# Kernel optimization log

Hardware: AMD Instinct MI355X
Metric: run time of the kernel (lower is better)

Reference implementation:

```python
import jax, jax.numpy as jnp
from jax import lax
import numpy as np

B, L, D = 2, 2048, 768
DI, DS, DTR, K = 1536, 16, 48, 4  # d_inner, d_state, dt_rank, d_conv
EPS = 1e-5


def layernorm(x, g, b):
    mu = jnp.mean(x, axis=-1, keepdims=True)
    var = jnp.mean(jnp.square(x - mu), axis=-1, keepdims=True)
    return (x - mu) * lax.rsqrt(var + EPS) * g + b


def mamba(x, in_w, conv_w, conv_b, xproj_w, dt_w, dt_b, A_log, Dp, out_w):
    # x: [B, L, D]
    xz = x @ in_w.T                       # [B, L, 2*DI]
    xc, z = jnp.split(xz, 2, axis=-1)     # [B, L, DI] each
    # causal depthwise conv1d, kernel K, left pad K-1, truncate to L
    xp = jnp.pad(xc, ((0, 0), (K - 1, 0), (0, 0)))
    conv = conv_b + sum(xp[:, k:k + L, :] * conv_w[:, k] for k in range(K))
    xc = jax.nn.silu(conv)
    dbc = xc @ xproj_w.T                  # [B, L, DTR+2*DS]
    dt = dbc[..., :DTR]
    Bm = dbc[..., DTR:DTR + DS]           # [B, L, DS]
    Cm = dbc[..., DTR + DS:]              # [B, L, DS]
    dt = jax.nn.softplus(dt @ dt_w.T + dt_b)  # [B, L, DI]
    A = -jnp.exp(A_log)                   # [DI, DS]

    def step(h, inp):
        dt_t, B_t, C_t, x_t = inp         # [B,DI], [B,DS], [B,DS], [B,DI]
        dA = jnp.exp(dt_t[..., None] * A)               # [B, DI, DS]
        h = dA * h + (dt_t * x_t)[..., None] * B_t[:, None, :]
        y = jnp.einsum('bds,bs->bd', h, C_t)
        return h, y

    h0 = jnp.zeros((x.shape[0], DI, DS), x.dtype)
    _, ys = lax.scan(step, h0, (dt.transpose(1, 0, 2), Bm.transpose(1, 0, 2),
                                Cm.transpose(1, 0, 2), xc.transpose(1, 0, 2)))
    y = ys.transpose(1, 0, 2) + xc * Dp   # [B, L, DI]
    y = y * jax.nn.silu(z)
    return y @ out_w.T                    # [B, L, D]


def setup_inputs() -> dict:
    key = jax.random.key(0)
    ks = iter(jax.random.split(key, 40))
    r = lambda s, sc=0.02: jax.random.normal(next(ks), s, jnp.float32) * sc
    A0 = jnp.log(jnp.broadcast_to(jnp.arange(1, DS + 1, dtype=jnp.float32), (DI, DS)))
    def mamba_params(p):
        return {
            f'{p}_in_w': r((2 * DI, D)), f'{p}_conv_w': r((DI, K), 0.2),
            f'{p}_conv_b': jnp.zeros((DI,)), f'{p}_xproj_w': r((DTR + 2 * DS, DI)),
            f'{p}_dt_w': r((DI, DTR), 0.1), f'{p}_dt_b': jnp.zeros((DI,)),
            f'{p}_A_log': A0, f'{p}_D': jnp.ones((DI,)), f'{p}_out_w': r((D, DI)),
        }
    inp = {'x': jax.random.normal(next(ks), (B, L, D), jnp.float32),
           'norm_g': jnp.ones((D,)), 'norm_b': jnp.zeros((D,))}
    inp.update(mamba_params('f'))
    inp.update(mamba_params('b'))
    inp.update({'mix_w': r((D, 2 * D)), 'mix_b': jnp.zeros((D,)),
                'ffn_w1': r((4 * D, D)), 'ffn_b1': jnp.zeros((4 * D,)),
                'ffn_w2': r((D, 4 * D)), 'ffn_b2': jnp.zeros((D,)),
                'ffn_norm_g': jnp.ones((D,)), 'ffn_norm_b': jnp.zeros((D,))})
    return inp


def reference(x, norm_g, norm_b,
              f_in_w, f_conv_w, f_conv_b, f_xproj_w, f_dt_w, f_dt_b, f_A_log, f_D, f_out_w,
              b_in_w, b_conv_w, b_conv_b, b_xproj_w, b_dt_w, b_dt_b, b_A_log, b_D, b_out_w,
              mix_w, mix_b, ffn_w1, ffn_b1, ffn_w2, ffn_b2, ffn_norm_g, ffn_norm_b):
    residual = x
    xn = layernorm(x, norm_g, norm_b)
    xf = mamba(xn, f_in_w, f_conv_w, f_conv_b, f_xproj_w, f_dt_w, f_dt_b, f_A_log, f_D, f_out_w)
    xb = mamba(jnp.flip(xn, axis=1), b_in_w, b_conv_w, b_conv_b, b_xproj_w,
               b_dt_w, b_dt_b, b_A_log, b_D, b_out_w)
    xb = jnp.flip(xb, axis=1)
    xm = jnp.concatenate([xf, xb], axis=-1) @ mix_w.T + mix_b
    h = xm + residual
    hn = layernorm(h, ffn_norm_g, ffn_norm_b)
    ff = jax.nn.gelu(hn @ ffn_w1.T + ffn_b1) @ ffn_w2.T + ffn_b2  # dropout = eval identity
    return ff + h
```

## Files before the change

kernel.cpp:

```cpp
#include <hip/hip_runtime.h>
#include <hip/hip_bf16.h>
#include <math.h>

#define NB 2
#define LL 2048
#define DD 768
#define DI 1536
#define DS 16
#define MM (NB*LL)
#define TCH 64
#define NCH 32

typedef __hip_bfloat16 bf16;
typedef __attribute__((ext_vector_type(8))) __bf16 bf16x8;
typedef __attribute__((ext_vector_type(4))) float f32x4;

__device__ __forceinline__ float b2f(bf16 v){ return __bfloat162float(v); }
__device__ __forceinline__ bf16 f2b(float v){ return __float2bfloat16(v); }

__device__ __forceinline__ void un2(unsigned u, float& lo, float& hi){
  union {unsigned i; float f;} a, b;
  a.i = u << 16; b.i = u & 0xffff0000u;
  lo = a.f; hi = b.f;
}

__device__ __forceinline__ void async_cp16(const bf16* g, __bf16* l) {
  __builtin_amdgcn_global_load_lds((const __attribute__((address_space(1))) void*)g,
                                   (__attribute__((address_space(3))) void*)l, 16, 0, 0);
}

#define ACT_NONE 0
#define ACT_SOFTPLUS 1
#define ACT_GELU 2

__device__ __forceinline__ float apply_act(float v, int act) {
  if (act == ACT_SOFTPLUS) {
    v = (v > 15.f) ? v : log1pf(__expf(v));
  } else if (act == ACT_GELU) {
    float u = 0.7978845608028654f * (v + 0.044715f*v*v*v);
    v = 0.5f * v * (1.f + tanhf(u));
  }
  return v;
}

__global__ void gemm_kernel(const bf16* __restrict__ A, int lda,
                            const bf16* __restrict__ B, int ldb,
                            void* __restrict__ C, int ldc,
                            int N, int K,
                            const float* __restrict__ bias,
                            const float* __restrict__ addp, int ldadd,
                            int act, int f32out)
{
  __shared__ __bf16 As[128*64];
  __shared__ __bf16 Bs[128*64];
  const int tid  = threadIdx.x;
  const int lane = tid & 63, wave = tid >> 6;
  const int m0 = blockIdx.x * 128, n0 = blockIdx.y * 128;
  const int wm = wave & 1, wn = wave >> 1;

  const int srow = wave*32 + (lane >> 3);
  const int gsw  = (lane & 7) ^ ((lane >> 3) & 7);
  const int scol = gsw * 8;
  const bf16* Ag[4]; const bf16* Bg[4];
  __bf16 *AsW[4], *BsW[4];
  #pragma unroll
  for (int i = 0; i < 4; i++) {
    int ar = m0 + srow + i*8;
    Ag[i] = A + (size_t)ar * lda + scol;
    int br = n0 + srow + i*8; if (br > N-1) br = N-1;
    Bg[i] = B + (size_t)br * ldb + scol;
    AsW[i] = &As[(wave*32 + i*8)*64];
    BsW[i] = &Bs[(wave*32 + i*8)*64];
  }

  f32x4 acc[4][4] = {};
  const int arow = wm*64 + (lane & 15);
  const int brow = wn*64 + (lane & 15);
  const int rx = lane & 7;
  const int gq = lane >> 4;

  for (int kb = 0; kb < K; kb += 64) {
    __syncthreads();
    #pragma unroll
    for (int i = 0; i < 4; i++) {
      async_cp16(Ag[i] + kb, AsW[i]);
      async_cp16(Bg[i] + kb, BsW[i]);
    }
    __syncthreads();
    #pragma unroll
    for (int h = 0; h < 2; h++) {
      const int kk = ((h*4 + gq) ^ rx) * 8;
      bf16x8 af[4], bfr[4];
      #pragma unroll
      for (int i = 0; i < 4; i++) af[i]  = *(const bf16x8*)&As[(arow + i*16)*64 + kk];
      #pragma unroll
      for (int j = 0; j < 4; j++) bfr[j] = *(const bf16x8*)&Bs[(brow + j*16)*64 + kk];
      #pragma unroll
      for (int i = 0; i < 4; i++)
        #pragma unroll
        for (int j = 0; j < 4; j++)
          acc[i][j] = __builtin_amdgcn_mfma_f32_16x16x32_bf16(af[i], bfr[j], acc[i][j], 0, 0, 0);
    }
  }

  bf16*  Cb = (bf16*)C;
  float* Cf = (float*)C;
  #pragma unroll
  for (int i = 0; i < 4; i++) {
    int rbase = m0 + wm*64 + i*16 + (lane >> 4)*4;
    #pragma unroll
    for (int j = 0; j < 4; j++) {
      int col = n0 + wn*64 + j*16 + (lane & 15);
      if (col >= N) continue;
      float bv = bias ? bias[col] : 0.f;
      #pragma unroll
      for (int r = 0; r < 4; r++) {
        int row = rbase + r;
        float v = apply_act(acc[i][j][r] + bv, act);
        if (addp) v += addp[(size_t)row * ldadd + col];
        if (f32out) Cf[(size_t)row * ldc + col] = v;
        else        Cb[(size_t)row * ldc + col] = f2b(v);
      }
    }
  }
}

__global__ void gemm64_kernel(const bf16* __restrict__ A, int lda, size_t sA,
                              const bf16* __restrict__ B, int ldb, size_t sB,
                              void* __restrict__ C, int ldc, size_t sC,
                              int N, int K,
                              const float* __restrict__ bias0,
                              const float* __restrict__ bias1, int biasBase,
                              const float* __restrict__ addp, int ldadd,
                              int act, int f32out)
{
  __shared__ __bf16 As[64*64];
  __shared__ __bf16 Bs[64*64];
  const int tid  = threadIdx.x;
  const int lane = tid & 63, wave = tid >> 6;
  const int z = blockIdx.z;
  A += (size_t)z * sA;
  B += (size_t)z * sB;
  const float* bias = ((biasBase + z) ? bias1 : bias0);
  const int m0 = blockIdx.x * 64, n0 = blockIdx.y * 64;
  const int wm = wave & 1, wn = wave >> 1;

  const int srow = wave*16 + (lane >> 3);
  const int gsw  = (lane & 7) ^ ((lane >> 3) & 7);
  const int scol = gsw * 8;
  const bf16* Ag[2]; const bf16* Bg[2];
  __bf16 *AsW[2], *BsW[2];
  #pragma unroll
  for (int i = 0; i < 2; i++) {
    int ar = m0 + srow + i*8;
    Ag[i] = A + (size_t)ar * lda + scol;
    int br = n0 + srow + i*8; if (br > N-1) br = N-1;
    Bg[i] = B + (size_t)br * ldb + scol;
    AsW[i] = &As[(wave*16 + i*8)*64];
    BsW[i] = &Bs[(wave*16 + i*8)*64];
  }

  f32x4 acc[2][2] = {};
  const int arow = wm*32 + (lane & 15);
  const int brow = wn*32 + (lane & 15);
  const int rx = lane & 7;
  const int gq = lane >> 4;

  for (int kb = 0; kb < K; kb += 64) {
    __syncthreads();
    #pragma unroll
    for (int i = 0; i < 2; i++) {
      async_cp16(Ag[i] + kb, AsW[i]);
      async_cp16(Bg[i] + kb, BsW[i]);
    }
    __syncthreads();
    #pragma unroll
    for (int h = 0; h < 2; h++) {
      const int kk = ((h*4 + gq) ^ rx) * 8;
      bf16x8 af[2], bfr[2];
      #pragma unroll
      for (int i = 0; i < 2; i++) af[i]  = *(const bf16x8*)&As[(arow + i*16)*64 + kk];
      #pragma unroll
      for (int j = 0; j < 2; j++) bfr[j] = *(const bf16x8*)&Bs[(brow + j*16)*64 + kk];
      #pragma unroll
      for (int i = 0; i < 2; i++)
        #pragma unroll
        for (int j = 0; j < 2; j++)
          acc[i][j] = __builtin_amdgcn_mfma_f32_16x16x32_bf16(af[i], bfr[j], acc[i][j], 0, 0, 0);
    }
  }

  bf16*  Cb = (bf16*)C + z*sC;
  float* Cf = (float*)C + z*sC;
  #pragma unroll
  for (int i = 0; i < 2; i++) {
    int rbase = m0 + wm*32 + i*16 + (lane >> 4)*4;
    #pragma unroll
    for (int j = 0; j < 2; j++) {
      int col = n0 + wn*32 + j*16 + (lane & 15);
      if (col >= N) continue;
      float bv = bias ? bias[col] : 0.f;
      #pragma unroll
      for (int r = 0; r < 4; r++) {
        int row = rbase + r;
        float v = apply_act(acc[i][j][r] + bv, act);
        if (addp) v += addp[(size_t)row * ldadd + col];
        if (f32out) Cf[(size_t)row * ldc + col] = v;
        else        Cb[(size_t)row * ldc + col] = f2b(v);
      }
    }
  }
}

__global__ void ln_kernel(const float* __restrict__ x, const float* __restrict__ g,
                          const float* __restrict__ b, bf16* __restrict__ out)
{
  const int row = blockIdx.x;
  const int tid = threadIdx.x;
  const float* xr = x + (size_t)row * DD;
  float v[3], s = 0.f, s2 = 0.f;
  #pragma unroll
  for (int i = 0; i < 3; i++) {
    float f = xr[tid + i*256];
    v[i] = f; s += f; s2 += f*f;
  }
  #pragma unroll
  for (int o = 32; o > 0; o >>= 1) { s += __shfl_down(s, o, 64); s2 += __shfl_down(s2, o, 64); }
  __shared__ float ps[4], ps2[4];
  int wave = tid >> 6;
  if ((tid & 63) == 0) { ps[wave] = s; ps2[wave] = s2; }
  __syncthreads();
  s = ps[0]+ps[1]+ps[2]+ps[3]; s2 = ps2[0]+ps2[1]+ps2[2]+ps2[3];
  float mu = s * (1.f/DD);
  float var = s2 * (1.f/DD) - mu*mu;
  float rs = rsqrtf(var + 1e-5f);
  #pragma unroll
  for (int i = 0; i < 3; i++) {
    int c = tid + i*256;
    float o = (v[i] - mu) * rs * g[c] + b[c];
    out[(size_t)row * DD + c] = f2b(o);
  }
}

__global__ void conv_silu_kernel(const bf16* __restrict__ xz, int ldxz, int xzDirOff,
                                 const float* __restrict__ cw0, const float* __restrict__ cb0,
                                 const float* __restrict__ cw1, const float* __restrict__ cb1,
                                 bf16* __restrict__ xc, size_t sXc, int dirBase)
{
  int idx = blockIdx.x * 256 + threadIdx.x;
  int sIdx = (idx >= DI) ? 1 : 0;
  int d = idx - sIdx*DI;
  int dir = dirBase + sIdx;
  int row = blockIdx.y;
  int b = row >> 11, t = row & 2047;
  const float* cw = dir ? cw1 : cw0;
  const float* cb = dir ? cb1 : cb0;
  float acc = cb[d];
  float w0 = cw[d*4+0], w1 = cw[d*4+1], w2 = cw[d*4+2], w3 = cw[d*4+3];
  const bf16* base = xz + (size_t)(b*2048) * ldxz + sIdx*xzDirOff + d;
  if (dir == 0) {
    if (t >= 3) acc += b2f(base[(size_t)(t-3)*ldxz]) * w0;
    if (t >= 2) acc += b2f(base[(size_t)(t-2)*ldxz]) * w1;
    if (t >= 1) acc += b2f(base[(size_t)(t-1)*ldxz]) * w2;
    acc += b2f(base[(size_t)t*ldxz]) * w3;
  } else {
    if (t <= 2044) acc += b2f(base[(size_t)(t+3)*ldxz]) * w0;
    if (t <= 2045) acc += b2f(base[(size_t)(t+2)*ldxz]) * w1;
    if (t <= 2046) acc += b2f(base[(size_t)(t+1)*ldxz]) * w2;
    acc += b2f(base[(size_t)t*ldxz]) * w3;
  }
  float y = acc / (1.f + __expf(-acc));
  xc[sIdx*sXc + (size_t)row * DI + d] = f2b(y);
}

#define SZ_INW (2*DI*DD)
#define SZ_XP  (80*DI)
#define SZ_OUT (DD*DI)
#define SZ_DTW (DI*64)
#define SZ_AN  (DI*16)
#define SZ_MIX (2*DD*DD)
#define SZ_F1  (4*DD*DD)
__global__ void prep_all_kernel(const float* fi, const float* bi,
                                const float* fxp, const float* bxp,
                                const float* fo, const float* bo,
                                const float* fdt, const float* bdt,
                                const float* fa, const float* ba,
                                const float* mw, const float* f1, const float* f2,
                                bf16* w_in, bf16* w_xp2, bf16* w_out2, bf16* dtwp2,
                                float* An2, bf16* w_mix, bf16* w_f1, bf16* w_f2)
{
  int i = blockIdx.x * 256 + threadIdx.x;
  if (i < SZ_INW) { w_in[i] = f2b(fi[i]); return; }               i -= SZ_INW;
  if (i < SZ_INW) { w_in[SZ_INW + i] = f2b(bi[i]); return; }      i -= SZ_INW;
  if (i < SZ_XP)  { w_xp2[i] = f2b(fxp[i]); return; }             i -= SZ_XP;
  if (i < SZ_XP)  { w_xp2[SZ_XP + i] = f2b(bxp[i]); return; }     i -= SZ_XP;
  if (i < SZ_OUT) { w_out2[i] = f2b(fo[i]); return; }             i -= SZ_OUT;
  if (i < SZ_OUT) { w_out2[SZ_OUT + i] = f2b(bo[i]); return; }    i -= SZ_OUT;
  if (i < SZ_DTW) { int r=i>>6,c=i&63; dtwp2[i] = (c<48)?f2b(fdt[r*48+c]):f2b(0.f); return; } i -= SZ_DTW;
  if (i < SZ_DTW) { int r=i>>6,c=i&63; dtwp2[SZ_DTW+i] = (c<48)?f2b(bdt[r*48+c]):f2b(0.f); return; } i -= SZ_DTW;
  if (i < SZ_AN)  { int d=i>>4,s=i&15; An2[s*DI+d] = -__expf(fa[i]); return; } i -= SZ_AN;
  if (i < SZ_AN)  { int d=i>>4,s=i&15; An2[SZ_AN + s*DI+d] = -__expf(ba[i]); return; } i -= SZ_AN;
  if (i < SZ_MIX) { w_mix[i] = f2b(mw[i]); return; }              i -= SZ_MIX;
  if (i < SZ_F1)  { w_f1[i] = f2b(f1[i]); return; }               i -= SZ_F1;
  w_f2[i] = f2b(f2[i]);
}

__global__ void scan_partial(const bf16* __restrict__ dt, size_t sDt,
                             const bf16* __restrict__ xc, size_t sXc,
                             const bf16* __restrict__ dbc, size_t sDbc,
                             const float* __restrict__ An, size_t sAn,
                             float* __restrict__ Pp, float* __restrict__ Sp,
                             int dirBase)
{
  const int tid = threadIdx.x;
  const int sIdx = blockIdx.z >> 1, b = blockIdx.z & 1;
  const int dir = dirBase + sIdx;
  const int c = blockIdx.y;
  const int d = blockIdx.x * 256 + tid;
  dt  += sIdx*sDt; xc += sIdx*sXc; dbc += sIdx*sDbc;
  const int rowbase = b*2048 + c*TCH;
  __shared__ unsigned bcs[TCH*16];
  for (int i = tid; i < TCH*16; i += 256) {
    int r = i >> 4, dw = i & 15;
    bcs[i] = ((const unsigned*)(dbc + (size_t)(rowbase + r)*96 + 48))[dw];
  }
  __syncthreads();
  float A[16], P[16], g[16];
  #pragma unroll
  for (int s = 0; s < 16; s++) { A[s] = An[sIdx*sAn + s*DI + d]; P[s] = 1.f; g[s] = 0.f; }
  int ph0 = dir ? (TCH-1) : 0;
  float dtv = b2f(dt[(size_t)(rowbase+ph0)*DI + d]);
  float xv  = b2f(xc[(size_t)(rowbase+ph0)*DI + d]);
  for (int t = 0; t < TCH; t++) {
    const int ph = dir ? (TCH-1-t) : t;
    const int tn = (t+1 < TCH) ? t+1 : t;
    const int phn = dir ? (TCH-1-tn) : tn;
    float dtn = b2f(dt[(size_t)(rowbase+phn)*DI + d]);
    float xvn = b2f(xc[(size_t)(rowbase+phn)*DI + d]);
    unsigned ub[8];
    *(uint4*)&ub[0] = *(const uint4*)&bcs[ph*16];
    *(uint4*)&ub[4] = *(const uint4*)&bcs[ph*16 + 4];
    float Bv[16];
    #pragma unroll
    for (int k = 0; k < 8; k++) un2(ub[k], Bv[2*k], Bv[2*k+1]);
    float u = dtv * xv;
    #pragma unroll
    for (int s = 0; s < 16; s++) {
      float dA = __expf(dtv * A[s]);
      P[s] *= dA;
      g[s] = dA * g[s] + u * Bv[s];
    }
    dtv = dtn; xv = xvn;
  }
  size_t base = ((((size_t)sIdx*NB + b)*NCH + c)*DI + d) * 16;
  #pragma unroll
  for (int s = 0; s < 16; s++) { Pp[base+s] = P[s]; Sp[base+s] = g[s]; }
}

__global__ void scan_combine(const float* __restrict__ Pp, const float* __restrict__ Sp,
                             float* __restrict__ h0, int dirBase)
{
  const int j = blockIdx.x * 256 + threadIdx.x;
  const int b = blockIdx.y;
  const int sIdx = blockIdx.z;
  const int dir = dirBase + sIdx;
  float h = 0.f;
  for (int k = 0; k < NCH; k++) {
    int c = dir ? (NCH-1-k) : k;
    size_t idx = (((size_t)sIdx*NB + b)*NCH + c)*DI*16 + j;
    h0[idx] = h;
    h = Pp[idx]*h + Sp[idx];
  }
}

__global__ void scan_final(const bf16* __restrict__ dt, size_t sDt,
                           const bf16* __restrict__ xc, size_t sXc,
                           const bf16* __restrict__ dbc, size_t sDbc,
                           const bf16* __restrict__ xz, int ldxz, int xzDirOff,
                           const float* __restrict__ An, size_t sAn,
                           const float* __restrict__ Dp0, const float* __restrict__ Dp1,
                           const float* __restrict__ h0,
                           bf16* __restrict__ yout, size_t sY, int dirBase)
{
  const int tid = threadIdx.x;
  const int sIdx = blockIdx.z >> 1, b = blockIdx.z & 1;
  const int dir = dirBase + sIdx;
  const int c = blockIdx.y;
  const int d = blockIdx.x * 256 + tid;
  dt += sIdx*sDt; xc += sIdx*sXc; dbc += sIdx*sDbc; yout += sIdx*sY;
  const float* Dp = dir ? Dp1 : Dp0;
  const int rowbase = b*2048 + c*TCH;
  __shared__ unsigned bcs[TCH*16];
  for (int i = tid; i < TCH*16; i += 256) {
    int r = i >> 4, dw = i & 15;
    bcs[i] = ((const unsigned*)(dbc + (size_t)(rowbase + r)*96 + 48))[dw];
  }
  __syncthreads();
  float A[16], h[16];
  size_t hbase = ((((size_t)sIdx*NB + b)*NCH + c)*DI + d) * 16;
  #pragma unroll
  for (int s = 0; s < 16; s++) { A[s] = An[sIdx*sAn + s*DI + d]; h[s] = h0[hbase+s]; }
  const float Dd = Dp[d];
  const bf16* zp = xz + sIdx*xzDirOff + DI + d;
  int ph0 = dir ? (TCH-1) : 0;
  float dtv = b2f(dt[(size_t)(rowbase+ph0)*DI + d]);
  float xv  = b2f(xc[(size_t)(rowbase+ph0)*DI + d]);
  float zv  = b2f(zp[(size_t)(rowbase+ph0)*ldxz]);
  for (int t = 0; t < TCH; t++) {
    const int ph = dir ? (TCH-1-t) : t;
    const int row = rowbase + ph;
    const int tn = (t+1 < TCH) ? t+1 : t;
    const int phn = dir ? (TCH-1-tn) : tn;
    float dtn = b2f(dt[(size_t)(rowbase+phn)*DI + d]);
    float xvn = b2f(xc[(size_t)(rowbase+phn)*DI + d]);
    float zvn = b2f(zp[(size_t)(rowbase+phn)*ldxz]);
    unsigned ub[8], uc[8];
    *(uint4*)&ub[0] = *(const uint4*)&bcs[ph*16];
    *(uint4*)&ub[4] = *(const uint4*)&bcs[ph*16 + 4];
    *(uint4*)&uc[0] = *(const uint4*)&bcs[ph*16 + 8];
    *(uint4*)&uc[4] = *(const uint4*)&bcs[ph*16 + 12];
    float Bv[16], Cv[16];
    #pragma unroll
    for (int k = 0; k < 8; k++) { un2(ub[k], Bv[2*k], Bv[2*k+1]); un2(uc[k], Cv[2*k], Cv[2*k+1]); }
    float u = dtv * xv;
    float y = 0.f;
    #pragma unroll
    for (int s = 0; s < 16; s++) {
      float dA = __expf(dtv * A[s]);
      h[s] = dA * h[s] + u * Bv[s];
      y += h[s] * Cv[s];
    }
    float yg = (y + xv * Dd) * (zv / (1.f + __expf(-zv)));
    yout[(size_t)row*DI + d] = f2b(yg);
    dtv = dtn; xv = xvn; zv = zvn;
  }
}

extern "C" void kernel_launch(void* const* d_in, const int* in_sizes, int n_in,
                              void* d_out, int out_size, void* d_ws, size_t ws_size,
                              hipStream_t stream)
{
  const float* x      = (const float*)d_in[0];
  const float* norm_g = (const float*)d_in[1];
  const float* norm_b = (const float*)d_in[2];
  const float* fi  = (const float*)d_in[3];
  const float* fcw = (const float*)d_in[4];
  const float* fcb = (const float*)d_in[5];
  const float* fxp = (const float*)d_in[6];
  const float* fdt = (const float*)d_in[7];
  const float* fdb = (const float*)d_in[8];
  const float* fa  = (const float*)d_in[9];
  const float* fD  = (const float*)d_in[10];
  const float* fo  = (const float*)d_in[11];
  const float* bi  = (const float*)d_in[12];
  const float* bcw = (const float*)d_in[13];
  const float* bcb = (const float*)d_in[14];
  const float* bxp = (const float*)d_in[15];
  const float* bdt = (const float*)d_in[16];
  const float* bdb = (const float*)d_in[17];
  const float* ba  = (const float*)d_in[18];
  const float* bD  = (const float*)d_in[19];
  const float* bo  = (const float*)d_in[20];
  const float* mix_w  = (const float*)d_in[21];
  const float* mix_b  = (const float*)d_in[22];
  const float* ffn_w1 = (const float*)d_in[23];
  const float* ffn_b1 = (const float*)d_in[24];
  const float* ffn_w2 = (const float*)d_in[25];
  const float* ffn_b2 = (const float*)d_in[26];
  const float* ffn_ng = (const float*)d_in[27];
  const float* ffn_nb = (const float*)d_in[28];

  auto al = [](size_t x){ return (x + 255) & ~(size_t)255; };
  const size_t fixedB =
      al((size_t)2*SZ_AN*4) + al((size_t)2*SZ_DTW*2) + al((size_t)2*SZ_INW*2) +
      al((size_t)2*SZ_XP*2) + al((size_t)2*SZ_OUT*2) + al((size_t)SZ_MIX*2) +
      al((size_t)SZ_F1*2) + al((size_t)SZ_F1*2) + al((size_t)MM*DD*2) + al((size_t)MM*DI*2);
  const size_t concB = fixedB + al((size_t)MM*2*DI*2*2) + 2*al((size_t)2*MM*DI*2) +
      al((size_t)2*MM*96*2) + 3*al((size_t)2*NB*NCH*DI*16*4);
  const bool conc = (ws_size >= concB);

  size_t o = 0;
  char* wsb = (char*)d_ws;
  auto nxt = [&](size_t bytes) -> char* {
    char* p = wsb + o; o += (bytes + 255) & ~(size_t)255; return p;
  };
  float* An2   = (float*)nxt((size_t)2*SZ_AN*4);
  bf16*  dtwp2 = (bf16*) nxt((size_t)2*SZ_DTW*2);
  bf16*  w_in  = (bf16*) nxt((size_t)2*SZ_INW*2);
  bf16*  w_xp2 = (bf16*) nxt((size_t)2*SZ_XP*2);
  bf16*  w_out2= (bf16*) nxt((size_t)2*SZ_OUT*2);
  bf16*  w_mix = (bf16*) nxt((size_t)SZ_MIX*2);
  bf16*  w_f1  = (bf16*) nxt((size_t)SZ_F1*2);
  bf16*  w_f2  = (bf16*) nxt((size_t)SZ_F1*2);
  bf16*  xn    = (bf16*) nxt((size_t)MM*DD*2);
  bf16*  xfb   = (bf16*) nxt((size_t)MM*DI*2);

  bf16 *xz, *xc, *dtb, *dbc;  float *Pp, *Sp, *h0, *hbuf;
  int ldxz, xzDirOff;
  size_t sXc, sDbc, sDt;
  if (conc) {
    xz  = (bf16*) nxt((size_t)MM*2*DI*2*2);
    xc  = (bf16*) nxt((size_t)2*MM*DI*2);
    dtb = (bf16*) nxt((size_t)2*MM*DI*2);
    dbc = (bf16*) nxt((size_t)2*MM*96*2);
    Pp  = (float*)nxt((size_t)2*NB*NCH*DI*16*4);
    Sp  = (float*)nxt((size_t)2*NB*NCH*DI*16*4);
    h0  = (float*)nxt((size_t)2*NB*NCH*DI*16*4);
    hbuf = Pp;
    ldxz = 2*2*DI; xzDirOff = 2*DI;
    sXc = (size_t)MM*DI; sDbc = (size_t)MM*96; sDt = (size_t)MM*DI;
  } else {
    xz  = (bf16*) nxt((size_t)MM*2*DI*2);
    xc  = (bf16*) nxt((size_t)MM*DI*2);
    dtb = (bf16*) nxt((size_t)MM*DI*2);
    dbc = (bf16*) nxt((size_t)MM*96*2);
    Pp  = (float*)nxt((size_t)NB*NCH*DI*16*4);
    Sp  = (float*)nxt((size_t)NB*NCH*DI*16*4);
    h0  = (float*)nxt((size_t)NB*NCH*DI*16*4);
    hbuf = (float*)dtb;
    ldxz = 2*DI; xzDirOff = 0;
    sXc = 0; sDbc = 0; sDt = 0;
  }
  bf16* hn = xn;
  bf16* a1 = xz;

  const int prepN = 2*SZ_INW + 2*SZ_XP + 2*SZ_OUT + 2*SZ_DTW + 2*SZ_AN + SZ_MIX + 2*SZ_F1;
  prep_all_kernel<<<(prepN + 255)/256, 256, 0, stream>>>(
      fi, bi, fxp, bxp, fo, bo, fdt, bdt, fa, ba, mix_w, ffn_w1, ffn_w2,
      w_in, w_xp2, w_out2, dtwp2, An2, w_mix, w_f1, w_f2);

  ln_kernel<<<MM, 256, 0, stream>>>(x, norm_g, norm_b, xn);

  if (conc) {
    gemm_kernel<<<dim3(32, 48), 256, 0, stream>>>(xn, DD, w_in, DD, xz, ldxz,
                                                  2*2*DI, DD, nullptr, nullptr, 0,
                                                  ACT_NONE, 0);
    conv_silu_kernel<<<dim3(12, MM), 256, 0, stream>>>(xz, ldxz, xzDirOff,
                                                       fcw, fcb, bcw, bcb, xc, sXc, 0);
    gemm64_kernel<<<dim3(64, 2, 2), 256, 0, stream>>>(xc, DI, sXc, w_xp2, DI, (size_t)SZ_XP,
                                                      dbc, 96, sDbc, 80, DI,
                                                      nullptr, nullptr, 0, nullptr, 0, ACT_NONE, 0);
    gemm64_kernel<<<dim3(64, 24, 2), 256, 0, stream>>>(dbc, 96, sDbc, dtwp2, 64, (size_t)SZ_DTW,
                                                       dtb, DI, sDt, DI, 64,
                                                       fdb, bdb, 0, nullptr, 0, ACT_SOFTPLUS, 0);
    scan_partial<<<dim3(DI/256, NCH, 4), 256, 0, stream>>>(dtb, sDt, xc, sXc, dbc, sDbc,
                                                           An2, (size_t)SZ_AN, Pp, Sp, 0);
    scan_combine<<<dim3(DI*16/256, NB, 2), 256, 0, stream>>>(Pp, Sp, h0, 0);
    scan_final<<<dim3(DI/256, NCH, 4), 256, 0, stream>>>(dtb, sDt, xc, sXc, dbc, sDbc,
                                                         xz, ldxz, xzDirOff, An2, (size_t)SZ_AN,
                                                         fD, bD, h0, xc, sXc, 0);
    gemm64_kernel<<<dim3(64, 12, 2), 256, 0, stream>>>(xc, DI, sXc, w_out2, DI, (size_t)SZ_OUT,
                                                       xfb, 2*DD, (size_t)DD, DD, DI,
                                                       nullptr, nullptr, 0, nullptr, 0, ACT_NONE, 0);
  } else {
    for (int dir = 0; dir < 2; ++dir) {
      gemm_kernel<<<dim3(32, 24), 256, 0, stream>>>(xn, DD, w_in + (size_t)dir*SZ_INW, DD,
                                                    xz, ldxz, 2*DI, DD, nullptr, nullptr, 0,
                                                    ACT_NONE, 0);
      conv_silu_kernel<<<dim3(6, MM), 256, 0, stream>>>(xz, ldxz, 0,
                                                        fcw, fcb, bcw, bcb, xc, 0, dir);
      gemm64_kernel<<<dim3(64, 2, 1), 256, 0, stream>>>(xc, DI, 0, w_xp2 + (size_t)dir*SZ_XP, DI, 0,
                                                        dbc, 96, 0, 80, DI,
                                                        nullptr, nullptr, 0, nullptr, 0, ACT_NONE, 0);
      gemm64_kernel<<<dim3(64, 24, 1), 256, 0, stream>>>(dbc, 96, 0, dtwp2 + (size_t)dir*SZ_DTW, 64, 0,
                                                         dtb, DI, 0, DI, 64,
                                                         fdb, bdb, dir, nullptr, 0, ACT_SOFTPLUS, 0);
      scan_partial<<<dim3(DI/256, NCH, 2), 256, 0, stream>>>(dtb, 0, xc, 0, dbc, 0,
                                                             An2 + (size_t)dir*SZ_AN, 0, Pp, Sp, dir);
      scan_combine<<<dim3(DI*16/256, NB, 1), 256, 0, stream>>>(Pp, Sp, h0, dir);
      scan_final<<<dim3(DI/256, NCH, 2), 256, 0, stream>>>(dtb, 0, xc, 0, dbc, 0,
                                                           xz, ldxz, 0, An2 + (size_t)dir*SZ_AN, 0,
                                                           fD, bD, h0, xc, 0, dir);
      gemm64_kernel<<<dim3(64, 12, 1), 256, 0, stream>>>(xc, DI, 0, w_out2 + (size_t)dir*SZ_OUT, DI, 0,
                                                         (void*)((bf16*)xfb + dir*DD), 2*DD, 0, DD, DI,
                                                         nullptr, nullptr, 0, nullptr, 0, ACT_NONE, 0);
    }
  }

  gemm64_kernel<<<dim3(64, 12, 1), 256, 0, stream>>>(xfb, 2*DD, 0, w_mix, 2*DD, 0,
                                                     hbuf, DD, 0, DD, 2*DD,
                                                     mix_b, mix_b, 0, x, DD, ACT_NONE, 1);
  ln_kernel<<<MM, 256, 0, stream>>>(hbuf, ffn_ng, ffn_nb, hn);
  gemm_kernel<<<dim3(32, 24), 256, 0, stream>>>(hn, DD, w_f1, DD, a1, 4*DD,
                                                4*DD, DD, ffn_b1, nullptr, 0, ACT_GELU, 0);
  gemm64_kernel<<<dim3(64, 12, 1), 256, 0, stream>>>(a1, 4*DD, 0, w_f2, 4*DD, 0,
                                                     d_out, DD, 0, DD, 4*DD,
                                                     ffn_b2, ffn_b2, 0, hbuf, DD, ACT_NONE, 1);
}
```

Measured before the change: 633.5 us.

## Fold out-projection into mix weights, widen GEMM to 8 waves, vectorize conv

Precomputes a combined weight by multiplying the mix weight with the transposed out-projection weights, so the two per-direction out-projection GEMMs plus the mix GEMM become a single GEMM over the gated scan output with K=3072. The main 128x128 GEMM now runs 512 threads with each wave owning a 64x32 sub-tile. The causal conv+SiLU kernel processes 8 rows per block with 8-wide bf16 vector loads and stores. The weight-folding GEMM runs on every call and adds workspace, and folding changes bf16 rounding order.

Measured after the change: 565.6 us. 1.12x faster.

```diff
diff --git a/kernel.cpp b/kernel.cpp
--- a/kernel.cpp
+++ b/kernel.cpp
@@ -10,6 +10,7 @@
 #define MM (NB*LL)
 #define TCH 64
 #define NCH 32
+#define CONV_R 8
 
 typedef __hip_bfloat16 bf16;
 typedef __attribute__((ext_vector_type(8))) __bf16 bf16x8;
@@ -17,6 +18,9 @@
 
 __device__ __forceinline__ float b2f(bf16 v){ return __bfloat162float(v); }
 __device__ __forceinline__ bf16 f2b(float v){ return __float2bfloat16(v); }
+__device__ __forceinline__ float bu2f(unsigned short u){
+  union {unsigned i; float f;} a; a.i = ((unsigned)u) << 16; return a.f;
+}
 
 __device__ __forceinline__ void un2(unsigned u, float& lo, float& hi){
   union {unsigned i; float f;} a, b;
@@ -43,62 +47,60 @@
   return v;
 }
 
-__global__ void gemm_kernel(const bf16* __restrict__ A, int lda,
-                            const bf16* __restrict__ B, int ldb,
-                            void* __restrict__ C, int ldc,
-                            int N, int K,
-                            const float* __restrict__ bias,
-                            const float* __restrict__ addp, int ldadd,
-                            int act, int f32out)
+__global__ __launch_bounds__(512)
+void gemm_kernel(const bf16* __restrict__ A, int lda,
+                 const bf16* __restrict__ B, int ldb,
+                 void* __restrict__ C, int ldc,
+                 int N, int K,
+                 const float* __restrict__ bias,
+                 const float* __restrict__ addp, int ldadd,
+                 int act, int f32out)
 {
   __shared__ __bf16 As[128*64];
   __shared__ __bf16 Bs[128*64];
   const int tid  = threadIdx.x;
   const int lane = tid & 63, wave = tid >> 6;
   const int m0 = blockIdx.x * 128, n0 = blockIdx.y * 128;
-  const int wm = wave & 1, wn = wave >> 1;
-
-  const int srow = wave*32 + (lane >> 3);
-  const int gsw  = (lane & 7) ^ ((lane >> 3) & 7);
+  const int wm = wave >> 2, wn = wave & 3;
+
+  const int srow = tid >> 3;
+  const int gsw  = (tid & 7) ^ (srow & 7);
   const int scol = gsw * 8;
-  const bf16* Ag[4]; const bf16* Bg[4];
-  __bf16 *AsW[4], *BsW[4];
-  #pragma unroll
-  for (int i = 0; i < 4; i++) {
-    int ar = m0 + srow + i*8;
-    Ag[i] = A + (size_t)ar * lda + scol;
-    int br = n0 + srow + i*8; if (br > N-1) br = N-1;
+  const bf16* Ag[2]; const bf16* Bg[2]; int dstv[2];
+  #pragma unroll
+  for (int i = 0; i < 2; i++) {
+    int r = srow + i*64;
+    Ag[i] = A + (size_t)(m0 + r) * lda + scol;
+    int br = n0 + r; if (br > N-1) br = N-1;
     Bg[i] = B + (size_t)br * ldb + scol;
-    AsW[i] = &As[(wave*32 + i*8)*64];
-    BsW[i] = &Bs[(wave*32 + i*8)*64];
-  }
-
-  f32x4 acc[4][4] = {};
-  const int arow = wm*64 + (lane & 15);
-  const int brow = wn*64 + (lane & 15);
-  const int rx = lane & 7;
-  const int gq = lane >> 4;
+    dstv[i] = r*64 + (tid & 7)*8;
+  }
+
+  f32x4 acc[4][2] = {};
+  const int f = lane & 15, gq = lane >> 4, rx = lane & 7;
+  const int abase = wm*64;
+  const int bbase = wn*32;
 
   for (int kb = 0; kb < K; kb += 64) {
     __syncthreads();
     #pragma unroll
-    for (int i = 0; i < 4; i++) {
-      async_cp16(Ag[i] + kb, AsW[i]);
-      async_cp16(Bg[i] + kb, BsW[i]);
+    for (int i = 0; i < 2; i++) {
+      async_cp16(Ag[i] + kb, &As[dstv[i]]);
+      async_cp16(Bg[i] + kb, &Bs[dstv[i]]);
     }
     __syncthreads();
     #pragma unroll
     for (int h = 0; h < 2; h++) {
       const int kk = ((h*4 + gq) ^ rx) * 8;
-      bf16x8 af[4], bfr[4];
-      #pragma unroll
-      for (int i = 0; i < 4; i++) af[i]  = *(const bf16x8*)&As[(arow + i*16)*64 + kk];
-      #pragma unroll
-      for (int j = 0; j < 4; j++) bfr[j] = *(const bf16x8*)&Bs[(brow + j*16)*64 + kk];
+      bf16x8 af[4], bfr[2];
+      #pragma unroll
+      for (int i = 0; i < 4; i++) af[i]  = *(const bf16x8*)&As[(abase + i*16 + f)*64 + kk];
+      #pragma unroll
+      for (int j = 0; j < 2; j++) bfr[j] = *(const bf16x8*)&Bs[(bbase + j*16 + f)*64 + kk];
       #pragma unroll
       for (int i = 0; i < 4; i++)
         #pragma unroll
-        for (int j = 0; j < 4; j++)
+        for (int j = 0; j < 2; j++)
           acc[i][j] = __builtin_amdgcn_mfma_f32_16x16x32_bf16(af[i], bfr[j], acc[i][j], 0, 0, 0);
     }
   }
@@ -107,10 +109,10 @@
   float* Cf = (float*)C;
   #pragma unroll
   for (int i = 0; i < 4; i++) {
-    int rbase = m0 + wm*64 + i*16 + (lane >> 4)*4;
-    #pragma unroll
-    for (int j = 0; j < 4; j++) {
-      int col = n0 + wn*64 + j*16 + (lane & 15);
+    int rbase = m0 + wm*64 + i*16 + gq*4;
+    #pragma unroll
+    for (int j = 0; j < 2; j++) {
+      int col = n0 + wn*32 + j*16 + f;
       if (col >= N) continue;
       float bv = bias ? bias[col] : 0.f;
       #pragma unroll
@@ -247,30 +249,47 @@
                                  const float* __restrict__ cw1, const float* __restrict__ cb1,
                                  bf16* __restrict__ xc, size_t sXc, int dirBase)
 {
-  int idx = blockIdx.x * 256 + threadIdx.x;
-  int sIdx = (idx >= DI) ? 1 : 0;
-  int d = idx - sIdx*DI;
-  int dir = dirBase + sIdx;
-  int row = blockIdx.y;
-  int b = row >> 11, t = row & 2047;
+  const int tid = threadIdx.x;
+  const int sIdx = tid / 192;
+  const int lane8 = tid - sIdx*192;
+  const int d8 = lane8 * 8;
+  const int dir = dirBase + sIdx;
   const float* cw = dir ? cw1 : cw0;
   const float* cb = dir ? cb1 : cb0;
-  float acc = cb[d];
-  float w0 = cw[d*4+0], w1 = cw[d*4+1], w2 = cw[d*4+2], w3 = cw[d*4+3];
-  const bf16* base = xz + (size_t)(b*2048) * ldxz + sIdx*xzDirOff + d;
-  if (dir == 0) {
-    if (t >= 3) acc += b2f(base[(size_t)(t-3)*ldxz]) * w0;
-    if (t >= 2) acc += b2f(base[(size_t)(t-2)*ldxz]) * w1;
-    if (t >= 1) acc += b2f(base[(size_t)(t-1)*ldxz]) * w2;
-    acc += b2f(base[(size_t)t*ldxz]) * w3;
-  } else {
-    if (t <= 2044) acc += b2f(base[(size_t)(t+3)*ldxz]) * w0;
-    if (t <= 2045) acc += b2f(base[(size_t)(t+2)*ldxz]) * w1;
-    if (t <= 2046) acc += b2f(base[(size_t)(t+1)*ldxz]) * w2;
-    acc += b2f(base[(size_t)t*ldxz]) * w3;
-  }
-  float y = acc / (1.f + __expf(-acc));
-  xc[sIdx*sXc + (size_t)row * DI + d] = f2b(y);
+  float w[4][8], bb[8];
+  #pragma unroll
+  for (int j = 0; j < 8; j++) {
+    float4 wj = *(const float4*)&cw[(d8+j)*4];
+    w[0][j] = wj.x; w[1][j] = wj.y; w[2][j] = wj.z; w[3][j] = wj.w;
+    bb[j] = cb[d8+j];
+  }
+  const int r0 = blockIdx.x * CONV_R;
+  const int b = r0 >> 11, t0 = r0 & 2047;
+  const bf16* base = xz + (size_t)(b*2048)*ldxz + (size_t)sIdx*xzDirOff + d8;
+  bf16* out = xc + sIdx*sXc + (size_t)r0*DI + d8;
+  for (int rr = 0; rr < CONV_R; rr++) {
+    const int t = t0 + rr;
+    float acc[8];
+    #pragma unroll
+    for (int j = 0; j < 8; j++) acc[j] = bb[j];
+    #pragma unroll
+    for (int k = 0; k < 4; k++) {
+      int tt = dir ? (t + 3 - k) : (t - 3 + k);
+      if (tt >= 0 && tt <= 2047) {
+        union { bf16x8 v; unsigned short u[8]; } iv;
+        iv.v = *(const bf16x8*)(base + (size_t)tt*ldxz);
+        #pragma unroll
+        for (int j = 0; j < 8; j++) acc[j] += bu2f(iv.u[j]) * w[k][j];
+      }
+    }
+    union { bf16x8 v; bf16 e[8]; } o;
+    #pragma unroll
+    for (int j = 0; j < 8; j++) {
+      float y = acc[j] / (1.f + __expf(-acc[j]));
+      o.e[j] = f2b(y);
+    }
+    *(bf16x8*)(out + (size_t)rr*DI) = o.v;
+  }
 }
 
 #define SZ_INW (2*DI*DD)
@@ -286,8 +305,8 @@
                                 const float* fdt, const float* bdt,
                                 const float* fa, const float* ba,
                                 const float* mw, const float* f1, const float* f2,
-                                bf16* w_in, bf16* w_xp2, bf16* w_out2, bf16* dtwp2,
-                                float* An2, bf16* w_mix, bf16* w_f1, bf16* w_f2)
+                                bf16* w_in, bf16* w_xp2, bf16* w_out2, bf16* w_outT,
+                                bf16* dtwp2, float* An2, bf16* w_mix, bf16* w_f1, bf16* w_f2)
 {
   int i = blockIdx.x * 256 + threadIdx.x;
   if (i < SZ_INW) { w_in[i] = f2b(fi[i]); return; }               i -= SZ_INW;
@@ -296,6 +315,8 @@
   if (i < SZ_XP)  { w_xp2[SZ_XP + i] = f2b(bxp[i]); return; }     i -= SZ_XP;
   if (i < SZ_OUT) { w_out2[i] = f2b(fo[i]); return; }             i -= SZ_OUT;
   if (i < SZ_OUT) { w_out2[SZ_OUT + i] = f2b(bo[i]); return; }    i -= SZ_OUT;
+  if (i < SZ_OUT) { int k=i/768, p=i-k*768; w_outT[i] = f2b(fo[p*DI + k]); return; } i -= SZ_OUT;
+  if (i < SZ_OUT) { int k=i/768, p=i-k*768; w_outT[SZ_OUT + i] = f2b(bo[p*DI + k]); return; } i -= SZ_OUT;
   if (i < SZ_DTW) { int r=i>>6,c=i&63; dtwp2[i] = (c<48)?f2b(fdt[r*48+c]):f2b(0.f); return; } i -= SZ_DTW;
   if (i < SZ_DTW) { int r=i>>6,c=i&63; dtwp2[SZ_DTW+i] = (c<48)?f2b(bdt[r*48+c]):f2b(0.f); return; } i -= SZ_DTW;
   if (i < SZ_AN)  { int d=i>>4,s=i&15; An2[s*DI+d] = -__expf(fa[i]); return; } i -= SZ_AN;
@@ -380,7 +401,7 @@
                            const float* __restrict__ An, size_t sAn,
                            const float* __restrict__ Dp0, const float* __restrict__ Dp1,
                            const float* __restrict__ h0,
-                           bf16* __restrict__ yout, size_t sY, int dirBase)
+                           bf16* __restrict__ yout, int ldY, size_t sY, int dirBase)
 {
   const int tid = threadIdx.x;
   const int sIdx = blockIdx.z >> 1, b = blockIdx.z & 1;
@@ -431,7 +452,7 @@
       y += h[s] * Cv[s];
     }
     float yg = (y + xv * Dd) * (zv / (1.f + __expf(-zv)));
-    yout[(size_t)row*DI + d] = f2b(yg);
+    yout[(size_t)row*ldY + d] = f2b(yg);
     dtv = dtn; xv = xvn; zv = zvn;
   }
 }
@@ -473,10 +494,12 @@
   auto al = [](size_t x){ return (x + 255) & ~(size_t)255; };
   const size_t fixedB =
       al((size_t)2*SZ_AN*4) + al((size_t)2*SZ_DTW*2) + al((size_t)2*SZ_INW*2) +
-      al((size_t)2*SZ_XP*2) + al((size_t)2*SZ_OUT*2) + al((size_t)SZ_MIX*2) +
-      al((size_t)SZ_F1*2) + al((size_t)SZ_F1*2) + al((size_t)MM*DD*2) + al((size_t)MM*DI*2);
+      al((size_t)2*SZ_XP*2) + al((size_t)2*SZ_OUT*2) + al((size_t)2*SZ_OUT*2) +
+      al((size_t)SZ_MIX*2) + al((size_t)SZ_F1*2) + al((size_t)SZ_F1*2) +
+      al((size_t)MM*DD*2) + al((size_t)MM*DI*2);
   const size_t concB = fixedB + al((size_t)MM*2*DI*2*2) + 2*al((size_t)2*MM*DI*2) +
-      al((size_t)2*MM*96*2) + 3*al((size_t)2*NB*NCH*DI*16*4);
+      al((size_t)2*MM*96*2) + 3*al((size_t)2*NB*NCH*DI*16*4) +
+      al((size_t)MM*2*DI*2) + al((size_t)DD*2*DI*2);
   const bool conc = (ws_size >= concB);
 
   size_t o = 0;
@@ -489,13 +512,15 @@
   bf16*  w_in  = (bf16*) nxt((size_t)2*SZ_INW*2);
   bf16*  w_xp2 = (bf16*) nxt((size_t)2*SZ_XP*2);
   bf16*  w_out2= (bf16*) nxt((size_t)2*SZ_OUT*2);
+  bf16*  w_outT= (bf16*) nxt((size_t)2*SZ_OUT*2);
   bf16*  w_mix = (bf16*) nxt((size_t)SZ_MIX*2);
   bf16*  w_f1  = (bf16*) nxt((size_t)SZ_F1*2);
   bf16*  w_f2  = (bf16*) nxt((size_t)SZ_F1*2);
   bf16*  xn    = (bf16*) nxt((size_t)MM*DD*2);
   bf16*  xfb   = (bf16*) nxt((size_t)MM*DI*2);
 
-  bf16 *xz, *xc, *dtb, *dbc;  float *Pp, *Sp, *h0, *hbuf;
+  bf16 *xz, *xc, *dtb, *dbc, *ybuf = nullptr, *Gp = nullptr;
+  float *Pp, *Sp, *h0, *hbuf;
   int ldxz, xzDirOff;
   size_t sXc, sDbc, sDt;
   if (conc) {
@@ -506,6 +531,8 @@
     Pp  = (float*)nxt((size_t)2*NB*NCH*DI*16*4);
     Sp  = (float*)nxt((size_t)2*NB*NCH*DI*16*4);
     h0  = (float*)nxt((size_t)2*NB*NCH*DI*16*4);
+    ybuf= (bf16*) nxt((size_t)MM*2*DI*2);
+    Gp  = (bf16*) nxt((size_t)DD*2*DI*2);
     hbuf = Pp;
     ldxz = 2*2*DI; xzDirOff = 2*DI;
     sXc = (size_t)MM*DI; sDbc = (size_t)MM*96; sDt = (size_t)MM*DI;
@@ -524,19 +551,26 @@
   bf16* hn = xn;
   bf16* a1 = xz;
 
-  const int prepN = 2*SZ_INW + 2*SZ_XP + 2*SZ_OUT + 2*SZ_DTW + 2*SZ_AN + SZ_MIX + 2*SZ_F1;
+  const int prepN = 2*SZ_INW + 2*SZ_XP + 4*SZ_OUT + 2*SZ_DTW + 2*SZ_AN + SZ_MIX + 2*SZ_F1;
   prep_all_kernel<<<(prepN + 255)/256, 256, 0, stream>>>(
       fi, bi, fxp, bxp, fo, bo, fdt, bdt, fa, ba, mix_w, ffn_w1, ffn_w2,
-      w_in, w_xp2, w_out2, dtwp2, An2, w_mix, w_f1, w_f2);
+      w_in, w_xp2, w_out2, w_outT, dtwp2, An2, w_mix, w_f1, w_f2);
+
+  if (conc) {
+    gemm64_kernel<<<dim3(12, 24, 2), 256, 0, stream>>>(w_mix, 2*DD, (size_t)DD,
+                                                       w_outT, DD, (size_t)SZ_OUT,
+                                                       Gp, 2*DI, (size_t)DI, DI, DD,
+                                                       nullptr, nullptr, 0, nullptr, 0, ACT_NONE, 0);
+  }
 
   ln_kernel<<<MM, 256, 0, stream>>>(x, norm_g, norm_b, xn);
 
   if (conc) {
-    gemm_kernel<<<dim3(32, 48), 256, 0, stream>>>(xn, DD, w_in, DD, xz, ldxz,
+    gemm_kernel<<<dim3(32, 48), 512, 0, stream>>>(xn, DD, w_in, DD, xz, ldxz,
                                                   2*2*DI, DD, nullptr, nullptr, 0,
                                                   ACT_NONE, 0);
-    conv_silu_kernel<<<dim3(12, MM), 256, 0, stream>>>(xz, ldxz, xzDirOff,
-                                                       fcw, fcb, bcw, bcb, xc, sXc, 0);
+    conv_silu_kernel<<<MM/CONV_R, 384, 0, stream>>>(xz, ldxz, xzDirOff,
+                                                    fcw, fcb, bcw, bcb, xc, sXc, 0);
     gemm64_kernel<<<dim3(64, 2, 2), 256, 0, stream>>>(xc, DI, sXc, w_xp2, DI, (size_t)SZ_XP,
                                                       dbc, 96, sDbc, 80, DI,
                                                       nullptr, nullptr, 0, nullptr, 0, ACT_NONE, 0);
@@ -548,17 +582,17 @@
     scan_combine<<<dim3(DI*16/256, NB, 2), 256, 0, stream>>>(Pp, Sp, h0, 0);
     scan_final<<<dim3(DI/256, NCH, 4), 256, 0, stream>>>(dtb, sDt, xc, sXc, dbc, sDbc,
                                                          xz, ldxz, xzDirOff, An2, (size_t)SZ_AN,
-                                                         fD, bD, h0, xc, sXc, 0);
-    gemm64_kernel<<<dim3(64, 12, 2), 256, 0, stream>>>(xc, DI, sXc, w_out2, DI, (size_t)SZ_OUT,
-                                                       xfb, 2*DD, (size_t)DD, DD, DI,
-                                                       nullptr, nullptr, 0, nullptr, 0, ACT_NONE, 0);
+                                                         fD, bD, h0, ybuf, 2*DI, (size_t)DI, 0);
+    gemm64_kernel<<<dim3(64, 12, 1), 256, 0, stream>>>(ybuf, 2*DI, 0, Gp, 2*DI, 0,
+                                                       hbuf, DD, 0, DD, 2*DI,
+                                                       mix_b, mix_b, 0, x, DD, ACT_NONE, 1);
   } else {
     for (int dir = 0; dir < 2; ++dir) {
-      gemm_kernel<<<dim3(32, 24), 256, 0, stream>>>(xn, DD, w_in + (size_t)dir*SZ_INW, DD,
+      gemm_kernel<<<dim3(32, 24), 512, 0, stream>>>(xn, DD, w_in + (size_t)dir*SZ_INW, DD,
                                                     xz, ldxz, 2*DI, DD, nullptr, nullptr, 0,
                                                     ACT_NONE, 0);
-      conv_silu_kernel<<<dim3(6, MM), 256, 0, stream>>>(xz, ldxz, 0,
-                                                        fcw, fcb, bcw, bcb, xc, 0, dir);
+      conv_silu_kernel<<<MM/CONV_R, 192, 0, stream>>>(xz, ldxz, 0,
+                                                      fcw, fcb, bcw, bcb, xc, 0, dir);
       gemm64_kernel<<<dim3(64, 2, 1), 256, 0, stream>>>(xc, DI, 0, w_xp2 + (size_t)dir*SZ_XP, DI, 0,
                                                         dbc, 96, 0, 80, DI,
                                                         nullptr, nullptr, 0, nullptr, 0, ACT_NONE, 0);
@@ -570,18 +604,18 @@
       scan_combine<<<dim3(DI*16/256, NB, 1), 256, 0, stream>>>(Pp, Sp, h0, dir);
       scan_final<<<dim3(DI/256, NCH, 2), 256, 0, stream>>>(dtb, 0, xc, 0, dbc, 0,
                                                            xz, ldxz, 0, An2 + (size_t)dir*SZ_AN, 0,
-                                                           fD, bD, h0, xc, 0, dir);
+                                                           fD, bD, h0, xc, DI, 0, dir);
       gemm64_kernel<<<dim3(64, 12, 1), 256, 0, stream>>>(xc, DI, 0, w_out2 + (size_t)dir*SZ_OUT, DI, 0,
                                                          (void*)((bf16*)xfb + dir*DD), 2*DD, 0, DD, DI,
                                                          nullptr, nullptr, 0, nullptr, 0, ACT_NONE, 0);
     }
-  }
-
-  gemm64_kernel<<<dim3(64, 12, 1), 256, 0, stream>>>(xfb, 2*DD, 0, w_mix, 2*DD, 0,
-                                                     hbuf, DD, 0, DD, 2*DD,
-                                                     mix_b, mix_b, 0, x, DD, ACT_NONE, 1);
+    gemm64_kernel<<<dim3(64, 12, 1), 256, 0, stream>>>(xfb, 2*DD, 0, w_mix, 2*DD, 0,
+                                                       hbuf, DD, 0, DD, 2*DD,
+                                                       mix_b, mix_b, 0, x, DD, ACT_NONE, 1);
+  }
+
   ln_kernel<<<MM, 256, 0, stream>>>(hbuf, ffn_ng, ffn_nb, hn);
-  gemm_kernel<<<dim3(32, 24), 256, 0, stream>>>(hn, DD, w_f1, DD, a1, 4*DD,
+  gemm_kernel<<<dim3(32, 24), 512, 0, stream>>>(hn, DD, w_f1, DD, a1, 4*DD,
                                                 4*DD, DD, ffn_b1, nullptr, 0, ACT_GELU, 0);
   gemm64_kernel<<<dim3(64, 12, 1), 256, 0, stream>>>(a1, 4*DD, 0, w_f2, 4*DD, 0,
                                                      d_out, DD, 0, DD, 4*DD,
```
